# Kernel optimization log

Measured on AMD Instinct MI355X. Metric: run time of the kernel, lower is better.

The kernel has to match this reference:

```python
import jax, jax.numpy as jnp
import numpy as np

N = 100000   # nodes
E = 600000   # edges per sign
IN = 128     # in_dim
HID = 128    # hidden_dim
H = 8        # num_heads
D = HID // H # per-head out_feats = 16
OUT = 64     # out_dim
NEG_SLOPE = 0.2


def setup_inputs() -> dict:
    key = jax.random.key(0)
    ks = jax.random.split(key, 20)
    inp = {}
    inp['features'] = jax.random.normal(ks[0], (N, IN), dtype=jnp.float32)
    inp['pos_src'] = jax.random.randint(ks[1], (E,), 0, N, dtype=jnp.int32)
    inp['pos_dst'] = jax.random.randint(ks[2], (E,), 0, N, dtype=jnp.int32)
    inp['neg_src'] = jax.random.randint(ks[3], (E,), 0, N, dtype=jnp.int32)
    inp['neg_dst'] = jax.random.randint(ks[4], (E,), 0, N, dtype=jnp.int32)
    # GATConv params (DGL: fc weight, attn_l, attn_r, bias) for pos and neg convs
    s = 0.1
    inp['W_pos'] = jax.random.normal(ks[5], (IN, H * D), dtype=jnp.float32) * s
    inp['al_pos'] = jax.random.normal(ks[6], (H, D), dtype=jnp.float32) * s
    inp['ar_pos'] = jax.random.normal(ks[7], (H, D), dtype=jnp.float32) * s
    inp['b_pos'] = jnp.zeros((H * D,), dtype=jnp.float32)
    inp['W_neg'] = jax.random.normal(ks[8], (IN, H * D), dtype=jnp.float32) * s
    inp['al_neg'] = jax.random.normal(ks[9], (H, D), dtype=jnp.float32) * s
    inp['ar_neg'] = jax.random.normal(ks[10], (H, D), dtype=jnp.float32) * s
    inp['b_neg'] = jnp.zeros((H * D,), dtype=jnp.float32)
    # final MLP: Linear(2*HID, HID) -> ReLU -> Linear(HID, OUT)
    inp['W1'] = jax.random.normal(ks[11], (2 * HID, HID), dtype=jnp.float32) * s
    inp['b1'] = jnp.zeros((HID,), dtype=jnp.float32)
    inp['W2'] = jax.random.normal(ks[12], (HID, OUT), dtype=jnp.float32) * s
    inp['b2'] = jnp.zeros((OUT,), dtype=jnp.float32)
    return inp


def gat_conv(features, src, dst, W, al, ar, b, n):
    # DGL GATConv (eval mode, no feat/attn dropout, no residual/activation)
    feat = (features @ W).reshape(n, H, D)            # [N,H,D]
    el = (feat * al).sum(-1)                          # [N,H]
    er = (feat * ar).sum(-1)                          # [N,H]
    e = jax.nn.leaky_relu(el[src] + er[dst], NEG_SLOPE)  # [E,H] per-edge logits
    # edge softmax over incoming edges of each dst node, per head
    m = jax.ops.segment_max(e, dst, num_segments=n)   # [N,H]
    ex = jnp.exp(e - m[dst])                          # [E,H]
    s = jax.ops.segment_sum(ex, dst, num_segments=n)  # [N,H]
    a = ex / s[dst]                                   # [E,H]
    rst = jax.ops.segment_sum(a[:, :, None] * feat[src], dst, num_segments=n)  # [N,H,D]
    return rst.reshape(n, H * D) + b


def reference(features, pos_src, pos_dst, neg_src, neg_dst,
              W_pos, al_pos, ar_pos, b_pos,
              W_neg, al_neg, ar_neg, b_neg,
              W1, b1, W2, b2):
    n = features.shape[0]
    h_pos = gat_conv(features, pos_src, pos_dst, W_pos, al_pos, ar_pos, b_pos, n)
    h_neg = gat_conv(features, neg_src, neg_dst, W_neg, al_neg, ar_neg, b_neg, n)
    h = jnp.concatenate([h_pos, h_neg], axis=1)       # [N, 2*HID]
    h_final = jnp.maximum(h @ W1 + b1, 0.0) @ W2 + b2  # [N, OUT]
    return (h_pos, h_neg, h_final)
```

## Files before the change

kernel.cpp:

```cpp
#include <hip/hip_runtime.h>

#define NEG_SLOPE 0.2f
#define CAP 32

typedef __attribute__((ext_vector_type(8))) short short8;
typedef __attribute__((ext_vector_type(4))) float floatx4;

__device__ __forceinline__ unsigned short f2bf(float f) {
    union { float f; unsigned u; } v; v.f = f;
    unsigned r = v.u + 0x7FFF + ((v.u >> 16) & 1);
    return (unsigned short)(r >> 16);
}
__device__ __forceinline__ float bf2f(unsigned short u) {
    return __uint_as_float(((unsigned)u) << 16);
}

__global__ void convert_w_kernel(const float* __restrict__ Wp, const float* __restrict__ Wn,
                                 const float* __restrict__ W1, const float* __restrict__ W2,
                                 unsigned short* __restrict__ Wcat, unsigned short* __restrict__ W1t,
                                 unsigned short* __restrict__ W2t) {
    int i = blockIdx.x * blockDim.x + threadIdx.x;
    if (i < 256 * 128) {
        int nr = i >> 7, k = i & 127;
        float v = (nr < 128) ? Wp[k * 128 + nr] : Wn[k * 128 + (nr - 128)];
        Wcat[i] = f2bf(v);
    } else if (i < 256 * 128 + 128 * 256) {
        int j = i - 256 * 128;
        int nr = j >> 8, k = j & 255;
        W1t[j] = f2bf(W1[k * 128 + nr]);
    } else if (i < 256 * 128 + 128 * 256 + 64 * 128) {
        int j = i - 256 * 128 - 128 * 256;
        int nr = j >> 7, k = j & 127;
        W2t[j] = f2bf(W2[k * 64 + nr]);
    }
}

template<int KDIM, int N, bool IN_F32, bool RELU, bool OUT_BF16, bool SPLIT>
__global__ __launch_bounds__(256)
void gemm_stream_kernel(const void* __restrict__ Av, const unsigned short* __restrict__ Wt,
                        const float* __restrict__ bias, void* __restrict__ outv, int n_rows) {
    constexpr int KS = KDIM / 32;
    constexpr int NT = N / 16;
    static_assert(N * KDIM * 2 <= 65536, "LDS budget");
    __shared__ __align__(16) unsigned short Bs[N * KDIM];
    const int tid = threadIdx.x;

    constexpr int CH = (N * KDIM) / 8;
    for (int i = tid; i < CH; i += 256) {
        int r = i / (KDIM / 8), c8 = i % (KDIM / 8);
        float4 v = *(const float4*)(Wt + (size_t)r * KDIM + c8 * 8);
        unsigned byt = ((unsigned)(r * KDIM + c8 * 8) << 1) ^ ((unsigned)(r & 7) << 4);
        *(float4*)((char*)Bs + byt) = v;
    }
    __syncthreads();

    const int lane = tid & 63;
    const int lrow = lane & 15;
    const int q = lane >> 4;
    const unsigned swz = (unsigned)(lrow & 7) << 4;
    const char* const Bsb = (const char*)Bs + lrow * (2 * KDIM);
    const int gw = blockIdx.x * 4 + (tid >> 6);
    const int nw = gridDim.x * 4;
    const int ntiles = n_rows >> 4;

    for (int t = gw; t < ntiles; t += nw) {
        const int arow = t * 16 + lrow;
        short8 af[KS];
        if (IN_F32) {
            const float* Af = (const float*)Av + (size_t)arow * KDIM + q * 8;
#pragma unroll
            for (int ks = 0; ks < KS; ++ks) {
                float4 va = *(const float4*)(Af + ks * 32);
                float4 vb = *(const float4*)(Af + ks * 32 + 4);
                unsigned short o[8];
                o[0] = f2bf(va.x); o[1] = f2bf(va.y); o[2] = f2bf(va.z); o[3] = f2bf(va.w);
                o[4] = f2bf(vb.x); o[5] = f2bf(vb.y); o[6] = f2bf(vb.z); o[7] = f2bf(vb.w);
                af[ks] = *(short8*)o;
            }
        } else {
            const unsigned short* Ab = (const unsigned short*)Av + (size_t)arow * KDIM + q * 8;
#pragma unroll
            for (int ks = 0; ks < KS; ++ks)
                af[ks] = *(const short8*)(Ab + ks * 32);
        }

        floatx4 acc[NT];
#pragma unroll
        for (int nt = 0; nt < NT; ++nt) acc[nt] = (floatx4){0.f, 0.f, 0.f, 0.f};

#pragma unroll
        for (int ks = 0; ks < KS; ++ks) {
            const char* bp = Bsb + (((unsigned)(ks * 64 + q * 16)) ^ swz);
#pragma unroll
            for (int nt = 0; nt < NT; ++nt) {
                short8 bf = *(const short8*)(bp + nt * (16 * 2 * KDIM));
                acc[nt] = __builtin_amdgcn_mfma_f32_16x16x32_bf16(af[ks], bf, acc[nt], 0, 0, 0);
            }
        }

#pragma unroll
        for (int nt = 0; nt < NT; ++nt) {
            const int cl = nt * 16 + lrow;
            const float bv = bias ? bias[cl] : 0.f;
#pragma unroll
            for (int r = 0; r < 4; ++r) {
                const int grow = t * 16 + q * 4 + r;
                float v = acc[nt][r] + bv;
                if (RELU) v = fmaxf(v, 0.f);
                if (SPLIT) {
                    unsigned short* op = (unsigned short*)outv +
                        ((nt >= NT / 2) ? (size_t)n_rows * (N / 2) : (size_t)0);
                    op[(size_t)grow * (N / 2) + (cl & (N / 2 - 1))] = f2bf(v);
                } else if (OUT_BF16) {
                    ((unsigned short*)outv)[(size_t)grow * N + cl] = f2bf(v);
                } else {
                    ((float*)outv)[(size_t)grow * N + cl] = v;
                }
            }
        }
    }
}

__global__ void eler_kernel(const unsigned short* __restrict__ featb,
                            const float* __restrict__ al_p, const float* __restrict__ ar_p,
                            const float* __restrict__ al_n, const float* __restrict__ ar_n,
                            float* __restrict__ el_p, float* __restrict__ er_p,
                            float* __restrict__ el_n, float* __restrict__ er_n, int n) {
    int idx = blockIdx.x * blockDim.x + threadIdx.x;
    if (idx >= 2 * n * 8) return;
    int h = idx & 7;
    bool neg = idx >= n * 8;
    const float* al = neg ? al_n : al_p;
    const float* ar = neg ? ar_n : ar_p;
    float* el = neg ? el_n : el_p;
    float* er = neg ? er_n : er_p;
    int local = neg ? idx - n * 8 : idx;
    const unsigned* fu = (const unsigned*)(featb + (size_t)idx * 16);
    float sl = 0.f, sr = 0.f;
#pragma unroll
    for (int q = 0; q < 8; ++q) {
        unsigned u = fu[q];
        float lo = __uint_as_float(u << 16);
        float hi = __uint_as_float(u & 0xFFFF0000u);
        sl += lo * al[h * 16 + q * 2] + hi * al[h * 16 + q * 2 + 1];
        sr += lo * ar[h * 16 + q * 2] + hi * ar[h * 16 + q * 2 + 1];
    }
    el[local] = sl; er[local] = sr;
}

__global__ void scatter_kernel(const int* __restrict__ pos_src, const int* __restrict__ pos_dst,
                               const int* __restrict__ neg_src, const int* __restrict__ neg_dst,
                               int* __restrict__ cnt, int* __restrict__ bkt_p, int* __restrict__ bkt_n,
                               int ne, int n) {
    int e = blockIdx.x * blockDim.x + threadIdx.x;
    if (e < ne) {
        int d = pos_dst[e];
        int p = atomicAdd(&cnt[d], 1);
        if (p < CAP) bkt_p[d * CAP + p] = pos_src[e];
    } else if (e < 2 * ne) {
        int j = e - ne;
        int d = neg_dst[j];
        int p = atomicAdd(&cnt[n + d], 1);
        if (p < CAP) bkt_n[d * CAP + p] = neg_src[j];
    }
}

__global__ __launch_bounds__(256)
void gat_gather_kernel(const int* __restrict__ cnt,
                       const int* __restrict__ bkt_p, const int* __restrict__ bkt_n,
                       const float* __restrict__ el_p, const float* __restrict__ er_p,
                       const float* __restrict__ el_n, const float* __restrict__ er_n,
                       const unsigned short* __restrict__ featb,
                       const float* __restrict__ b_pos, const float* __restrict__ b_neg,
                       float* __restrict__ out, unsigned short* __restrict__ hcatb, int n) {
    int node = (blockIdx.x * 256 + threadIdx.x) >> 6;
    int lane = threadIdx.x & 63;
    if (node >= n) return;
    const int neg = blockIdx.y;
    const int* bkt = neg ? bkt_n : bkt_p;
    const float* el = neg ? el_n : el_p;
    const float* er = neg ? er_n : er_p;
    const unsigned short* fb = featb + (size_t)(neg ? n : 0) * 128;
    const float* bias = neg ? b_neg : b_pos;
    float* o = out + (size_t)(neg ? n : 0) * 128;
    const int coloff = neg ? 128 : 0;

    const int h = lane >> 3;
    const float erh = er[(size_t)node * 8 + h];
    int deg = cnt[(neg ? n : 0) + node];
    if (deg > CAP) deg = CAP;
    float acc0 = 0.f, acc1 = 0.f, denom = 0.f;

#define GSTEP(S)  do {                                                         \
        float x_ = el[(size_t)(S) * 8 + h] + erh;                              \
        x_ = x_ < 0.f ? NEG_SLOPE * x_ : x_;                                   \
        float w_ = __expf(x_);                                                 \
        denom += w_;                                                           \
        ushort2 f_ = *(const ushort2*)(fb + (size_t)(S) * 128 + lane * 2);     \
        acc0 = fmaf(w_, bf2f(f_.x), acc0);                                     \
        acc1 = fmaf(w_, bf2f(f_.y), acc1);                                     \
    } while (0)

    int sid = (lane < deg) ? bkt[(size_t)node * CAP + lane] : 0;
    int j = 0;
    for (; j + 8 <= deg; j += 8) {
        int s0 = __shfl(sid, j),     s1 = __shfl(sid, j + 1);
        int s2 = __shfl(sid, j + 2), s3 = __shfl(sid, j + 3);
        int s4 = __shfl(sid, j + 4), s5 = __shfl(sid, j + 5);
        int s6 = __shfl(sid, j + 6), s7 = __shfl(sid, j + 7);
        GSTEP(s0); GSTEP(s1); GSTEP(s2); GSTEP(s3);
        GSTEP(s4); GSTEP(s5); GSTEP(s6); GSTEP(s7);
    }
    for (; j + 4 <= deg; j += 4) {
        int s0 = __shfl(sid, j), s1 = __shfl(sid, j + 1);
        int s2 = __shfl(sid, j + 2), s3 = __shfl(sid, j + 3);
        GSTEP(s0); GSTEP(s1); GSTEP(s2); GSTEP(s3);
    }
    for (; j + 2 <= deg; j += 2) {
        int s0 = __shfl(sid, j), s1 = __shfl(sid, j + 1);
        GSTEP(s0); GSTEP(s1);
    }
    for (; j < deg; ++j) {
        int s = __shfl(sid, j);
        GSTEP(s);
    }
#undef GSTEP

    float inv = denom > 0.f ? 1.f / denom : 0.f;
    float2 ov;
    ov.x = fmaf(acc0, inv, bias[lane * 2]);
    ov.y = fmaf(acc1, inv, bias[lane * 2 + 1]);
    *(float2*)(o + (size_t)node * 128 + lane * 2) = ov;
    ushort2 hb; hb.x = f2bf(ov.x); hb.y = f2bf(ov.y);
    *(ushort2*)(hcatb + (size_t)node * 256 + coloff + lane * 2) = hb;
}

extern "C" void kernel_launch(void* const* d_in, const int* in_sizes, int n_in,
                              void* d_out, int out_size, void* d_ws, size_t ws_size,
                              hipStream_t stream) {
    const float* features = (const float*)d_in[0];
    const int* pos_src = (const int*)d_in[1];
    const int* pos_dst = (const int*)d_in[2];
    const int* neg_src = (const int*)d_in[3];
    const int* neg_dst = (const int*)d_in[4];
    const float* W_pos  = (const float*)d_in[5];
    const float* al_pos = (const float*)d_in[6];
    const float* ar_pos = (const float*)d_in[7];
    const float* b_pos  = (const float*)d_in[8];
    const float* W_neg  = (const float*)d_in[9];
    const float* al_neg = (const float*)d_in[10];
    const float* ar_neg = (const float*)d_in[11];
    const float* b_neg  = (const float*)d_in[12];
    const float* W1 = (const float*)d_in[13];
    const float* b1 = (const float*)d_in[14];
    const float* W2 = (const float*)d_in[15];
    const float* b2 = (const float*)d_in[16];

    const int n  = in_sizes[0] / 128;
    const int ne = in_sizes[1];

    float* out  = (float*)d_out;
    float* hfin = out + (size_t)n * 256;

    unsigned short* featb = (unsigned short*)d_ws;
    unsigned short* mid   = featb;
    unsigned short* hcatb = featb + (size_t)2 * n * 128;
    float* el_pos = (float*)(hcatb + (size_t)n * 256);
    float* er_pos = el_pos + (size_t)n * 8;
    float* el_neg = er_pos + (size_t)n * 8;
    float* er_neg = el_neg + (size_t)n * 8;
    unsigned short* Wcat = (unsigned short*)(er_neg + (size_t)n * 8);
    unsigned short* W1t  = Wcat + 256 * 128;
    unsigned short* W2t  = W1t + 128 * 256;
    int* cnt     = (int*)(W2t + 64 * 128);
    int* bkt_pos = cnt + 2 * (size_t)n;
    int* bkt_neg = bkt_pos + (size_t)n * CAP;

    const int ge2 = (2 * ne + 255) / 256;

    convert_w_kernel<<<(73728 + 255) / 256, 256, 0, stream>>>(W_pos, W_neg, W1, W2, Wcat, W1t, W2t);

    hipMemsetAsync(cnt, 0, sizeof(int) * 2 * (size_t)n, stream);
    scatter_kernel<<<ge2, 256, 0, stream>>>(pos_src, pos_dst, neg_src, neg_dst,
                                            cnt, bkt_pos, bkt_neg, ne, n);

    gemm_stream_kernel<128, 256, true, false, true, true>
        <<<512, 256, 0, stream>>>(features, Wcat, nullptr, featb, n);

    eler_kernel<<<(2 * n * 8 + 255) / 256, 256, 0, stream>>>(featb, al_pos, ar_pos, al_neg, ar_neg,
                                                             el_pos, er_pos, el_neg, er_neg, n);

    gat_gather_kernel<<<dim3((n + 3) / 4, 2), 256, 0, stream>>>(cnt, bkt_pos, bkt_neg,
                                                                el_pos, er_pos, el_neg, er_neg,
                                                                featb, b_pos, b_neg, out, hcatb, n);

    gemm_stream_kernel<256, 128, false, true, true, false>
        <<<512, 256, 0, stream>>>(hcatb, W1t, b1, mid, n);
    gemm_stream_kernel<128, 64, false, false, false, false>
        <<<512, 256, 0, stream>>>(mid, W2t, b2, hfin, n);
}
```

Measured before the change: 502.8 us.

## Fuse edge bucket scatter into feature projection GEMM launch

Merges the edge-bucketing scatter kernel into the first projection GEMM by appending scatter blocks to the GEMM grid, so the two independent stages share one launch and can overlap on the GPU. The GEMM templates are simplified accordingly. The per-node GAT output store becomes a nontemporal store. The scatter blocks inherit the GEMM's 64 KB static LDS allocation, which may limit how many of them can be resident at once.

```diff
diff --git a/kernel.cpp b/kernel.cpp
--- a/kernel.cpp
+++ b/kernel.cpp
@@ -5,6 +5,7 @@
 
 typedef __attribute__((ext_vector_type(8))) short short8;
 typedef __attribute__((ext_vector_type(4))) float floatx4;
+typedef __attribute__((ext_vector_type(2))) float floatx2;
 
 __device__ __forceinline__ unsigned short f2bf(float f) {
     union { float f; unsigned u; } v; v.f = f;
@@ -35,9 +36,92 @@
     }
 }
 
-template<int KDIM, int N, bool IN_F32, bool RELU, bool OUT_BF16, bool SPLIT>
 __global__ __launch_bounds__(256)
-void gemm_stream_kernel(const void* __restrict__ Av, const unsigned short* __restrict__ Wt,
+void fused_gemm_scatter_kernel(const float* __restrict__ Af, const unsigned short* __restrict__ Wt,
+                               unsigned short* __restrict__ featb, int n_rows,
+                               const int* __restrict__ pos_src, const int* __restrict__ pos_dst,
+                               const int* __restrict__ neg_src, const int* __restrict__ neg_dst,
+                               int* __restrict__ cnt, int* __restrict__ bkt_p, int* __restrict__ bkt_n,
+                               int ne, int ngemm) {
+    constexpr int KDIM = 128, N = 256, KS = 4, NT = 16;
+    __shared__ __align__(16) unsigned short Bs[N * KDIM];
+    const int tid = threadIdx.x;
+
+    if ((int)blockIdx.x >= ngemm) {
+        int e = (blockIdx.x - ngemm) * 256 + tid;
+        if (e < ne) {
+            int d = pos_dst[e];
+            int p = atomicAdd(&cnt[d], 1);
+            if (p < CAP) bkt_p[d * CAP + p] = pos_src[e];
+        } else if (e < 2 * ne) {
+            int j = e - ne;
+            int d = neg_dst[j];
+            int p = atomicAdd(&cnt[n_rows + d], 1);
+            if (p < CAP) bkt_n[d * CAP + p] = neg_src[j];
+        }
+        return;
+    }
+
+    for (int i = tid; i < (N * KDIM) / 8; i += 256) {
+        int r = i / (KDIM / 8), c8 = i % (KDIM / 8);
+        float4 v = *(const float4*)(Wt + (size_t)r * KDIM + c8 * 8);
+        unsigned byt = ((unsigned)(r * KDIM + c8 * 8) << 1) ^ ((unsigned)(r & 7) << 4);
+        *(float4*)((char*)Bs + byt) = v;
+    }
+    __syncthreads();
+
+    const int lane = tid & 63;
+    const int lrow = lane & 15;
+    const int q = lane >> 4;
+    const unsigned swz = (unsigned)(lrow & 7) << 4;
+    const char* const Bsb = (const char*)Bs + lrow * (2 * KDIM);
+    const int gw = blockIdx.x * 4 + (tid >> 6);
+    const int nw = ngemm * 4;
+    const int ntiles = n_rows >> 4;
+
+    for (int t = gw; t < ntiles; t += nw) {
+        const int arow = t * 16 + lrow;
+        short8 af[KS];
+        const float* Ap = Af + (size_t)arow * KDIM + q * 8;
+#pragma unroll
+        for (int ks = 0; ks < KS; ++ks) {
+            float4 va = *(const float4*)(Ap + ks * 32);
+            float4 vb = *(const float4*)(Ap + ks * 32 + 4);
+            unsigned short o[8];
+            o[0] = f2bf(va.x); o[1] = f2bf(va.y); o[2] = f2bf(va.z); o[3] = f2bf(va.w);
+            o[4] = f2bf(vb.x); o[5] = f2bf(vb.y); o[6] = f2bf(vb.z); o[7] = f2bf(vb.w);
+            af[ks] = *(short8*)o;
+        }
+
+        floatx4 acc[NT];
+#pragma unroll
+        for (int nt = 0; nt < NT; ++nt) acc[nt] = (floatx4){0.f, 0.f, 0.f, 0.f};
+#pragma unroll
+        for (int ks = 0; ks < KS; ++ks) {
+            const char* bp = Bsb + (((unsigned)(ks * 64 + q * 16)) ^ swz);
+#pragma unroll
+            for (int nt = 0; nt < NT; ++nt) {
+                short8 bf = *(const short8*)(bp + nt * (16 * 2 * KDIM));
+                acc[nt] = __builtin_amdgcn_mfma_f32_16x16x32_bf16(af[ks], bf, acc[nt], 0, 0, 0);
+            }
+        }
+
+#pragma unroll
+        for (int nt = 0; nt < NT; ++nt) {
+            const int cl = nt * 16 + lrow;
+#pragma unroll
+            for (int r = 0; r < 4; ++r) {
+                const int grow = t * 16 + q * 4 + r;
+                unsigned short* op = featb + ((nt >= NT / 2) ? (size_t)n_rows * 128 : (size_t)0);
+                op[(size_t)grow * 128 + (cl & 127)] = f2bf(acc[nt][r]);
+            }
+        }
+    }
+}
+
+template<int KDIM, int N, bool RELU, bool OUT_BF16>
+__global__ __launch_bounds__(256)
+void gemm_stream_kernel(const unsigned short* __restrict__ Av, const unsigned short* __restrict__ Wt,
                         const float* __restrict__ bias, void* __restrict__ outv, int n_rows) {
     constexpr int KS = KDIM / 32;
     constexpr int NT = N / 16;
@@ -64,30 +148,15 @@
     const int ntiles = n_rows >> 4;
 
     for (int t = gw; t < ntiles; t += nw) {
-        const int arow = t * 16 + lrow;
+        const unsigned short* Ab = Av + (size_t)(t * 16 + lrow) * KDIM + q * 8;
         short8 af[KS];
-        if (IN_F32) {
-            const float* Af = (const float*)Av + (size_t)arow * KDIM + q * 8;
-#pragma unroll
-            for (int ks = 0; ks < KS; ++ks) {
-                float4 va = *(const float4*)(Af + ks * 32);
-                float4 vb = *(const float4*)(Af + ks * 32 + 4);
-                unsigned short o[8];
-                o[0] = f2bf(va.x); o[1] = f2bf(va.y); o[2] = f2bf(va.z); o[3] = f2bf(va.w);
-                o[4] = f2bf(vb.x); o[5] = f2bf(vb.y); o[6] = f2bf(vb.z); o[7] = f2bf(vb.w);
-                af[ks] = *(short8*)o;
-            }
-        } else {
-            const unsigned short* Ab = (const unsigned short*)Av + (size_t)arow * KDIM + q * 8;
-#pragma unroll
-            for (int ks = 0; ks < KS; ++ks)
-                af[ks] = *(const short8*)(Ab + ks * 32);
-        }
+#pragma unroll
+        for (int ks = 0; ks < KS; ++ks)
+            af[ks] = *(const short8*)(Ab + ks * 32);
 
         floatx4 acc[NT];
 #pragma unroll
         for (int nt = 0; nt < NT; ++nt) acc[nt] = (floatx4){0.f, 0.f, 0.f, 0.f};
-
 #pragma unroll
         for (int ks = 0; ks < KS; ++ks) {
             const char* bp = Bsb + (((unsigned)(ks * 64 + q * 16)) ^ swz);
@@ -101,21 +170,14 @@
 #pragma unroll
         for (int nt = 0; nt < NT; ++nt) {
             const int cl = nt * 16 + lrow;
-            const float bv = bias ? bias[cl] : 0.f;
+            const float bv = bias[cl];
 #pragma unroll
             for (int r = 0; r < 4; ++r) {
                 const int grow = t * 16 + q * 4 + r;
                 float v = acc[nt][r] + bv;
                 if (RELU) v = fmaxf(v, 0.f);
-                if (SPLIT) {
-                    unsigned short* op = (unsigned short*)outv +
-                        ((nt >= NT / 2) ? (size_t)n_rows * (N / 2) : (size_t)0);
-                    op[(size_t)grow * (N / 2) + (cl & (N / 2 - 1))] = f2bf(v);
-                } else if (OUT_BF16) {
-                    ((unsigned short*)outv)[(size_t)grow * N + cl] = f2bf(v);
-                } else {
-                    ((float*)outv)[(size_t)grow * N + cl] = v;
-                }
+                if (OUT_BF16) ((unsigned short*)outv)[(size_t)grow * N + cl] = f2bf(v);
+                else          ((float*)outv)[(size_t)grow * N + cl] = v;
             }
         }
     }
@@ -146,23 +208,6 @@
         sr += lo * ar[h * 16 + q * 2] + hi * ar[h * 16 + q * 2 + 1];
     }
     el[local] = sl; er[local] = sr;
-}
-
-__global__ void scatter_kernel(const int* __restrict__ pos_src, const int* __restrict__ pos_dst,
-                               const int* __restrict__ neg_src, const int* __restrict__ neg_dst,
-                               int* __restrict__ cnt, int* __restrict__ bkt_p, int* __restrict__ bkt_n,
-                               int ne, int n) {
-    int e = blockIdx.x * blockDim.x + threadIdx.x;
-    if (e < ne) {
-        int d = pos_dst[e];
-        int p = atomicAdd(&cnt[d], 1);
-        if (p < CAP) bkt_p[d * CAP + p] = pos_src[e];
-    } else if (e < 2 * ne) {
-        int j = e - ne;
-        int d = neg_dst[j];
-        int p = atomicAdd(&cnt[n + d], 1);
-        if (p < CAP) bkt_n[d * CAP + p] = neg_src[j];
-    }
 }
 
 __global__ __launch_bounds__(256)
@@ -227,10 +272,10 @@
 #undef GSTEP
 
     float inv = denom > 0.f ? 1.f / denom : 0.f;
-    float2 ov;
+    floatx2 ov;
     ov.x = fmaf(acc0, inv, bias[lane * 2]);
     ov.y = fmaf(acc1, inv, bias[lane * 2 + 1]);
-    *(float2*)(o + (size_t)node * 128 + lane * 2) = ov;
+    __builtin_nontemporal_store(ov, (floatx2*)(o + (size_t)node * 128 + lane * 2));
     ushort2 hb; hb.x = f2bf(ov.x); hb.y = f2bf(ov.y);
     *(ushort2*)(hcatb + (size_t)node * 256 + coloff + lane * 2) = hb;
 }
@@ -276,16 +321,15 @@
     int* bkt_pos = cnt + 2 * (size_t)n;
     int* bkt_neg = bkt_pos + (size_t)n * CAP;
 
-    const int ge2 = (2 * ne + 255) / 256;
+    const int NGEMM = 512;
+    const int gsc = (2 * ne + 255) / 256;
 
     convert_w_kernel<<<(73728 + 255) / 256, 256, 0, stream>>>(W_pos, W_neg, W1, W2, Wcat, W1t, W2t);
-
     hipMemsetAsync(cnt, 0, sizeof(int) * 2 * (size_t)n, stream);
-    scatter_kernel<<<ge2, 256, 0, stream>>>(pos_src, pos_dst, neg_src, neg_dst,
-                                            cnt, bkt_pos, bkt_neg, ne, n);
-
-    gemm_stream_kernel<128, 256, true, false, true, true>
-        <<<512, 256, 0, stream>>>(features, Wcat, nullptr, featb, n);
+
+    fused_gemm_scatter_kernel<<<NGEMM + gsc, 256, 0, stream>>>(
+        features, Wcat, featb, n,
+        pos_src, pos_dst, neg_src, neg_dst, cnt, bkt_pos, bkt_neg, ne, NGEMM);
 
     eler_kernel<<<(2 * n * 8 + 255) / 256, 256, 0, stream>>>(featb, al_pos, ar_pos, al_neg, ar_neg,
                                                              el_pos, er_pos, el_neg, er_neg, n);
@@ -294,8 +338,6 @@
                                                                 el_pos, er_pos, el_neg, er_neg,
                                                                 featb, b_pos, b_neg, out, hcatb, n);
 
-    gemm_stream_kernel<256, 128, false, true, true, false>
-        <<<512, 256, 0, stream>>>(hcatb, W1t, b1, mid, n);
-    gemm_stream_kernel<128, 64, false, false, false, false>
-        <<<512, 256, 0, stream>>>(mid, W2t, b2, hfin, n);
-}
+    gemm_stream_kernel<256, 128, true, true><<<512, 256, 0, stream>>>(hcatb, W1t, b1, mid, n);
+    gemm_stream_kernel<128, 64, false, false><<<512, 256, 0, stream>>>(mid, W2t, b2, hfin, n);
+}
```

Result: faster. 452.5 us (-10.0%).
